# Kernel tuning notes

Measured on AMD Instinct MI355X. Metric: run time of the kernel, lower is better.

## Reference

```python
import jax, jax.numpy as jnp
import numpy as np

B, S = 2, 512
HID, FEAT = 768, 256
H, W = 512, 512
NUM_CLASSES = 9
BN_EPS = 1e-5


def setup_inputs() -> dict:
    key = jax.random.key(0)
    ks = jax.random.split(key, 20)
    hidden_states = jax.random.normal(ks[0], (B, S, HID), dtype=jnp.float32)
    # bbox in LayoutLM 0..1000 space, guaranteed x2>x1, y2>y1 for realistic coverage
    x1 = jax.random.randint(ks[1], (B, S), 0, 880)
    y1 = jax.random.randint(ks[2], (B, S), 0, 880)
    bw = jax.random.randint(ks[3], (B, S), 8, 120)
    bh = jax.random.randint(ks[4], (B, S), 8, 120)
    bbox = jnp.stack([x1, y1, jnp.minimum(x1 + bw, 1000), jnp.minimum(y1 + bh, 1000)], axis=-1).astype(jnp.int32)
    attention_mask = jnp.ones((B, S), dtype=jnp.int32)
    w_init = lambda k, shp: jax.random.normal(k, shp, dtype=jnp.float32) * 0.02
    return {
        "hidden_states": hidden_states,
        "bbox": bbox,
        "attention_mask": attention_mask,
        "proj_w": w_init(ks[5], (HID, FEAT)),
        "proj_b": jnp.zeros((FEAT,), jnp.float32),
        "conv1_w": w_init(ks[6], (128, FEAT, 3, 3)),
        "conv1_b": jnp.zeros((128,), jnp.float32),
        "bn1_g": jnp.ones((128,), jnp.float32),
        "bn1_b": jnp.zeros((128,), jnp.float32),
        "bn1_m": jnp.zeros((128,), jnp.float32),
        "bn1_v": jnp.ones((128,), jnp.float32),
        "conv2_w": w_init(ks[7], (64, 128, 3, 3)),
        "conv2_b": jnp.zeros((64,), jnp.float32),
        "bn2_g": jnp.ones((64,), jnp.float32),
        "bn2_b": jnp.zeros((64,), jnp.float32),
        "bn2_m": jnp.zeros((64,), jnp.float32),
        "bn2_v": jnp.ones((64,), jnp.float32),
        "conv3_w": w_init(ks[8], (NUM_CLASSES, 64, 1, 1)),
        "conv3_b": jnp.zeros((NUM_CLASSES,), jnp.float32),
    }


def _conv(x, w, b, pad):
    y = jax.lax.conv_general_dilated(x, w, (1, 1), [(pad, pad), (pad, pad)],
                                     dimension_numbers=("NCHW", "OIHW", "NCHW"))
    return y + b[None, :, None, None]


def _bn(x, g, b, m, v):
    scale = g / jnp.sqrt(v + BN_EPS)
    return (x - m[None, :, None, None]) * scale[None, :, None, None] + b[None, :, None, None]


def reference(hidden_states, bbox, attention_mask, proj_w, proj_b,
              conv1_w, conv1_b, bn1_g, bn1_b, bn1_m, bn1_v,
              conv2_w, conv2_b, bn2_g, bn2_b, bn2_m, bn2_v,
              conv3_w, conv3_b):
    features = hidden_states @ proj_w + proj_b  # [B,S,FEAT]

    # integer pixel coords, matching int(x * dim / 1000) truncation for x >= 0
    x1 = jnp.maximum((bbox[..., 0] * W) // 1000, 0)
    y1 = jnp.maximum((bbox[..., 1] * H) // 1000, 0)
    x2 = jnp.minimum((bbox[..., 2] * W) // 1000, W - 1)
    y2 = jnp.minimum((bbox[..., 3] * H) // 1000, H - 1)
    valid = (attention_mask == 1) & (jnp.arange(S) >= 1) & (x2 > x1) & (y2 > y1)  # [B,S]

    rows = jnp.arange(H)
    cols = jnp.arange(W)
    rows_in = (rows[None, None, :] >= y1[..., None]) & (rows[None, None, :] < y2[..., None])  # [B,S,H]
    cols_in = (cols[None, None, :] >= x1[..., None]) & (cols[None, None, :] < x2[..., None])  # [B,S,W]

    # sequential priority scatter: later tokens overwrite earlier ones
    def step(winner, xs):
        r, c, v, i = xs  # r:[B,H] c:[B,W] v:[B] i:scalar
        cov = v[:, None, None] & (r[:, :, None] & c[:, None, :])
        return jnp.where(cov, i, winner), None

    winner0 = jnp.zeros((B, H, W), jnp.int32)  # 0 == empty (token 0 is never valid)
    xs = (rows_in.transpose(1, 0, 2), cols_in.transpose(1, 0, 2),
          valid.T, jnp.arange(S, dtype=jnp.int32))
    winner, _ = jax.lax.scan(step, winner0, xs)  # [B,H,W]

    idx = winner.reshape(B, H * W)
    fm = jnp.take_along_axis(features, idx[:, :, None], axis=1)  # [B,HW,FEAT]
    fm = jnp.where((idx > 0)[:, :, None], fm, 0.0)
    feature_map = fm.reshape(B, H, W, FEAT).transpose(0, 3, 1, 2)  # [B,FEAT,H,W]

    x = jax.nn.relu(_bn(_conv(feature_map, conv1_w, conv1_b, 1), bn1_g, bn1_b, bn1_m, bn1_v))
    x = jax.nn.relu(_bn(_conv(x, conv2_w, conv2_b, 1), bn2_g, bn2_b, bn2_m, bn2_v))
    logits = _conv(x, conv3_w, conv3_b, 0)  # [B,NUM_CLASSES,H,W]
    return logits
```

## Files before the change

### kernel.cpp

```cpp
#include <hip/hip_runtime.h>
#include <hip/hip_bf16.h>

typedef __bf16 bf16x8 __attribute__((ext_vector_type(8)));
typedef float f32x4 __attribute__((ext_vector_type(4)));

#define HH 512
#define WW 512
#define NC 9
#define LDSB 25344
#define W3_OFF 62208
#define B3_OFF 64512

static __device__ __forceinline__ ushort f2bf(float x) {
  union { float f; unsigned u; } c; c.f = x;
  unsigned r = c.u + 0x7FFFu + ((c.u >> 16) & 1u);
  return (ushort)(r >> 16);
}

__global__ __launch_bounds__(256) void proj_gemm_kernel(
    const float* __restrict__ hs, const float* __restrict__ pw,
    const float* __restrict__ pb, float* __restrict__ feat) {
  __shared__ float As[16 * 132];
  __shared__ float4 Bs4[2048];
  int tid = threadIdx.x;
  int r0 = blockIdx.x * 16;
  int n0 = blockIdx.y * 64;
  int r = tid >> 4;
  int c4 = (tid & 15) << 2;
  float4 acc = *(const float4*)(pb + n0 + c4);
  for (int k0 = 0; k0 < 768; k0 += 128) {
    __syncthreads();
    #pragma unroll
    for (int i = 0; i < 8; ++i) {
      int idx = tid + i * 256;
      As[(idx >> 7) * 132 + (idx & 127)] =
          hs[(size_t)(r0 + (idx >> 7)) * 768 + k0 + (idx & 127)];
    }
    #pragma unroll
    for (int i = 0; i < 8; ++i) {
      int idx = tid + i * 256;
      Bs4[idx] = *(const float4*)(pw + (size_t)(k0 + (idx >> 4)) * 256 + n0 + ((idx & 15) << 2));
    }
    __syncthreads();
    const float* ar = As + r * 132;
    #pragma unroll 8
    for (int k = 0; k < 128; ++k) {
      float a = ar[k];
      float4 bv = Bs4[(k << 4) + (c4 >> 2)];
      acc.x = fmaf(a, bv.x, acc.x); acc.y = fmaf(a, bv.y, acc.y);
      acc.z = fmaf(a, bv.z, acc.z); acc.w = fmaf(a, bv.w, acc.w);
    }
  }
  *(float4*)(feat + (size_t)(r0 + r) * 256 + n0 + c4) = acc;
}

__global__ __launch_bounds__(64) void scatter_kernel(
    const int* __restrict__ bbox, const int* __restrict__ amask,
    int* __restrict__ winner) {
  int token = blockIdx.x;
  int b = token >> 9, s = token & 511;
  if (s == 0) return;
  const int* bb = bbox + (size_t)token * 4;
  int x1 = (bb[0] * 512) / 1000; if (x1 < 0) x1 = 0;
  int y1 = (bb[1] * 512) / 1000; if (y1 < 0) y1 = 0;
  int x2 = (bb[2] * 512) / 1000; if (x2 > 511) x2 = 511;
  int y2 = (bb[3] * 512) / 1000; if (y2 > 511) y2 = 511;
  if (amask[token] != 1 || x2 <= x1 || y2 <= y1) return;
  int lane = threadIdx.x;
  for (int yy = y1; yy < y2; ++yy) {
    int rowbase = (b << 18) + (yy << 9);
    for (int xx = x1 + lane; xx < x2; xx += 64)
      atomicMax(&winner[rowbase + xx], s);
  }
}

__global__ __launch_bounds__(256) void w1r_kernel(
    const float* __restrict__ w1, float* __restrict__ w1r) {
  int idx = blockIdx.x * 256 + threadIdx.x;
  int ic = idx / 1152, rem = idx - ic * 1152;
  int tap = rem >> 7, oc = rem & 127;
  w1r[idx] = w1[(size_t)oc * 2304 + ic * 9 + tap];
}

__global__ __launch_bounds__(256) void gtab_gemm_kernel(
    const float* __restrict__ feat, const float* __restrict__ w1r,
    float* __restrict__ G) {
  __shared__ float As[16 * 132];
  __shared__ float4 Bs4[2048];
  int tid = threadIdx.x;
  int r0 = blockIdx.x * 16;
  int n0 = blockIdx.y * 64;
  int r = tid >> 4;
  int c4 = (tid & 15) << 2;
  float4 acc = make_float4(0.f, 0.f, 0.f, 0.f);
  for (int k0 = 0; k0 < 256; k0 += 128) {
    __syncthreads();
    #pragma unroll
    for (int i = 0; i < 8; ++i) {
      int idx = tid + i * 256;
      As[(idx >> 7) * 132 + (idx & 127)] =
          feat[(size_t)(r0 + (idx >> 7)) * 256 + k0 + (idx & 127)];
    }
    #pragma unroll
    for (int i = 0; i < 8; ++i) {
      int idx = tid + i * 256;
      Bs4[idx] = *(const float4*)(w1r + (size_t)(k0 + (idx >> 4)) * 1152 + n0 + ((idx & 15) << 2));
    }
    __syncthreads();
    const float* ar = As + r * 132;
    #pragma unroll 8
    for (int k = 0; k < 128; ++k) {
      float a = ar[k];
      float4 bv = Bs4[(k << 4) + (c4 >> 2)];
      acc.x = fmaf(a, bv.x, acc.x); acc.y = fmaf(a, bv.y, acc.y);
      acc.z = fmaf(a, bv.z, acc.z); acc.w = fmaf(a, bv.w, acc.w);
    }
  }
  int row = r0 + r;
  if ((row & 511) == 0) acc = make_float4(0.f, 0.f, 0.f, 0.f);
  *(float4*)(G + (size_t)row * 1152 + n0 + c4) = acc;
}

__global__ __launch_bounds__(256) void gall_kernel(
    const float* __restrict__ G, float* __restrict__ Gall) {
  int idx = blockIdx.x * 256 + threadIdx.x;
  int row = idx >> 7, oc = idx & 127;
  const float* gr = G + (size_t)row * 1152 + oc;
  float s = 0.f;
  #pragma unroll
  for (int t = 0; t < 9; ++t) s += gr[t * 128];
  Gall[idx] = s;
}

__global__ __launch_bounds__(256) void w2t_kernel(
    const float* __restrict__ w2, ushort* __restrict__ w2t) {
  int oc = blockIdx.x;
  for (int k = threadIdx.x; k < 1152; k += 256) {
    int tap = k >> 7, ic = k & 127;
    w2t[(size_t)oc * 1152 + k] = f2bf(w2[(size_t)oc * 1152 + ic * 9 + tap]);
  }
}

__global__ __launch_bounds__(256) void conv1_gather_kernel(
    const int* __restrict__ winner,
    const float* __restrict__ G, const float* __restrict__ Gall,
    const float* __restrict__ cb, const float* __restrict__ g,
    const float* __restrict__ bt, const float* __restrict__ m,
    const float* __restrict__ v,
    ushort* __restrict__ buf1, size_t bstride, int b0, int hstart) {
  __shared__ float sscl[128], sshf[128];
  int tid = threadIdx.x;
  if (tid < 128) {
    float s = g[tid] * rsqrtf(v[tid] + 1e-5f);
    sscl[tid] = s;
    sshf[tid] = (cb[tid] - m[tid]) * s + bt[tid];
  }
  __syncthreads();
  int b = b0 + blockIdx.z;
  int px = blockIdx.x * 256 + tid;
  int r = px >> 9, w = px & 511;
  int h = hstart + r;
  ushort* dst = buf1 + (size_t)blockIdx.z * bstride + (size_t)px * 128;
  if (h < 0 || h >= HH) {
    uint4 z = make_uint4(0, 0, 0, 0);
    #pragma unroll
    for (int j = 0; j < 16; ++j) *(uint4*)(dst + j * 8) = z;
    return;
  }
  const int* wb = winner + (b << 18);
  int win[9];
  #pragma unroll
  for (int ky = 0; ky < 3; ++ky)
    #pragma unroll
    for (int kx = 0; kx < 3; ++kx) {
      int hp = h - 1 + ky, wp = w - 1 + kx;
      int s = 0;
      if (hp >= 0 && hp < HH && wp >= 0 && wp < WW) s = wb[(hp << 9) + wp];
      win[ky * 3 + kx] = s;
    }
  bool alleq = true;
  #pragma unroll
  for (int t = 1; t < 9; ++t) alleq = alleq && (win[t] == win[0]);

  if (alleq) {
    const float4* gp = (const float4*)(Gall + ((((size_t)b << 9) + win[0]) << 7));
    #pragma unroll
    for (int o8 = 0; o8 < 16; ++o8) {
      float4 a0 = gp[o8 * 2], a1 = gp[o8 * 2 + 1];
      const float* sc = &sscl[o8 * 8];
      const float* sh = &sshf[o8 * 8];
      union { ushort us[8]; uint4 v4; } pk;
      pk.us[0] = f2bf(fmaxf(fmaf(a0.x, sc[0], sh[0]), 0.f));
      pk.us[1] = f2bf(fmaxf(fmaf(a0.y, sc[1], sh[1]), 0.f));
      pk.us[2] = f2bf(fmaxf(fmaf(a0.z, sc[2], sh[2]), 0.f));
      pk.us[3] = f2bf(fmaxf(fmaf(a0.w, sc[3], sh[3]), 0.f));
      pk.us[4] = f2bf(fmaxf(fmaf(a1.x, sc[4], sh[4]), 0.f));
      pk.us[5] = f2bf(fmaxf(fmaf(a1.y, sc[5], sh[5]), 0.f));
      pk.us[6] = f2bf(fmaxf(fmaf(a1.z, sc[6], sh[6]), 0.f));
      pk.us[7] = f2bf(fmaxf(fmaf(a1.w, sc[7], sh[7]), 0.f));
      *(uint4*)(dst + o8 * 8) = pk.v4;
    }
  } else {
    size_t off[9];
    #pragma unroll
    for (int t = 0; t < 9; ++t)
      off[t] = ((size_t)((b << 9) + win[t])) * 1152 + t * 128;
    #pragma unroll
    for (int o8 = 0; o8 < 16; ++o8) {
      float4 a0 = make_float4(0, 0, 0, 0), a1 = a0;
      #pragma unroll
      for (int t = 0; t < 9; ++t) {
        const float4* gp = (const float4*)(G + off[t] + o8 * 8);
        float4 g0 = gp[0], g1 = gp[1];
        a0.x += g0.x; a0.y += g0.y; a0.z += g0.z; a0.w += g0.w;
        a1.x += g1.x; a1.y += g1.y; a1.z += g1.z; a1.w += g1.w;
      }
      const float* sc = &sscl[o8 * 8];
      const float* sh = &sshf[o8 * 8];
      union { ushort us[8]; uint4 v4; } pk;
      pk.us[0] = f2bf(fmaxf(fmaf(a0.x, sc[0], sh[0]), 0.f));
      pk.us[1] = f2bf(fmaxf(fmaf(a0.y, sc[1], sh[1]), 0.f));
      pk.us[2] = f2bf(fmaxf(fmaf(a0.z, sc[2], sh[2]), 0.f));
      pk.us[3] = f2bf(fmaxf(fmaf(a0.w, sc[3], sh[3]), 0.f));
      pk.us[4] = f2bf(fmaxf(fmaf(a1.x, sc[4], sh[4]), 0.f));
      pk.us[5] = f2bf(fmaxf(fmaf(a1.y, sc[5], sh[5]), 0.f));
      pk.us[6] = f2bf(fmaxf(fmaf(a1.z, sc[6], sh[6]), 0.f));
      pk.us[7] = f2bf(fmaxf(fmaf(a1.w, sc[7], sh[7]), 0.f));
      *(uint4*)(dst + o8 * 8) = pk.v4;
    }
  }
}

__global__ __launch_bounds__(256) void conv2_mfma_kernel(
    const ushort* __restrict__ buf1, const ushort* __restrict__ w2t,
    const float* __restrict__ cb, const float* __restrict__ g,
    const float* __restrict__ bt, const float* __restrict__ m_,
    const float* __restrict__ v_,
    const float* __restrict__ w3, const float* __restrict__ b3,
    float* __restrict__ out, size_t bstride, int b0, int hs0, int SR) {
  __shared__ uint4 lds4[4035];
  char* smem = (char*)lds4;
  int tid = threadIdx.x;
  int w0 = blockIdx.x * 64;
  int oh0 = blockIdx.y * 4;
  int b = b0 + blockIdx.z;
  const ushort* B1 = buf1 + (size_t)blockIdx.z * bstride;
  int wv = tid >> 6, lane = tid & 63;
  int l15 = lane & 15, l4 = lane >> 4;

  float scl[4], shf[4];
  #pragma unroll
  for (int nf = 0; nf < 4; ++nf) {
    int oc = nf * 16 + l15;
    float s = g[oc] * rsqrtf(v_[oc] + 1e-5f);
    scl[nf] = s;
    shf[nf] = (cb[oc] - m_[oc]) * s + bt[oc];
  }

  int aaddr[4][3];
  #pragma unroll
  for (int mf = 0; mf < 4; ++mf)
    #pragma unroll
    for (int kx = 0; kx < 3; ++kx) {
      int col = mf * 16 + l15 + kx;
      aaddr[mf][kx] = wv * 4224 + (col << 6) + ((l4 << 4) ^ (((col >> 1) & 3) << 4));
    }
  int baddr[4];
  #pragma unroll
  for (int nf = 0; nf < 4; ++nf) {
    int n = nf * 16 + l15;
    baddr[nf] = LDSB + (n << 6) + ((l4 << 4) ^ (((n >> 1) & 3) << 4));
  }

  f32x4 acc[4][4];
  #pragma unroll
  for (int mf = 0; mf < 4; ++mf)
    #pragma unroll
    for (int nf = 0; nf < 4; ++nf)
      acc[mf][nf] = (f32x4){0.f, 0.f, 0.f, 0.f};

  int bn = tid >> 2, bslot = tid & 3;
  int bd = LDSB + (bn << 6) + ((bslot << 4) ^ (((bn >> 1) & 3) << 4));

  for (int chunk = 0; chunk < 4; ++chunk) {
    int ic0 = chunk * 32;
    __syncthreads();
    uint4 av0, av1, av2, av3, av4, av5, av6;
    int ad0, ad1, ad2, ad3, ad4, ad5, ad6 = 0;
    av6 = make_uint4(0, 0, 0, 0);
#define ADEC(II, AV, AD) { \
      int i_ = (II); int slot = i_ & 3; int q = i_ >> 2; \
      int r_ = (q * 993) >> 16; int c_ = q - r_ * 66; \
      int wg = w0 - 1 + c_; \
      AD = ((r_ * 66 + c_) << 6) + ((slot << 4) ^ (((c_ >> 1) & 3) << 4)); \
      AV = make_uint4(0, 0, 0, 0); \
      if (wg >= 0 && wg < 512) \
        AV = *(const uint4*)(B1 + ((((size_t)(oh0 + r_)) << 9) + wg) * 128 + ic0 + slot * 8); \
    }
    ADEC(tid, av0, ad0);
    ADEC(tid + 256, av1, ad1);
    ADEC(tid + 512, av2, ad2);
    ADEC(tid + 768, av3, ad3);
    ADEC(tid + 1024, av4, ad4);
    ADEC(tid + 1280, av5, ad5);
    if (tid < 48) ADEC(tid + 1536, av6, ad6);
#undef ADEC
    uint4 bv[9];
    const ushort* wsrc = w2t + (size_t)bn * 1152 + ic0 + bslot * 8;
    #pragma unroll
    for (int j = 0; j < 9; ++j) bv[j] = *(const uint4*)(wsrc + j * 128);

    *(uint4*)(smem + ad0) = av0;
    *(uint4*)(smem + ad1) = av1;
    *(uint4*)(smem + ad2) = av2;
    *(uint4*)(smem + ad3) = av3;
    *(uint4*)(smem + ad4) = av4;
    *(uint4*)(smem + ad5) = av5;
    if (tid < 48) *(uint4*)(smem + ad6) = av6;
    #pragma unroll
    for (int j = 0; j < 9; ++j) *(uint4*)(smem + bd + j * 4096) = bv[j];
    __syncthreads();

    #pragma unroll
    for (int ky = 0; ky < 3; ++ky) {
      #pragma unroll
      for (int kx = 0; kx < 3; ++kx) {
        const int tap = ky * 3 + kx;
        bf16x8 bf0 = *(const bf16x8*)(smem + baddr[0] + tap * 4096);
        bf16x8 bf1 = *(const bf16x8*)(smem + baddr[1] + tap * 4096);
        bf16x8 bf2 = *(const bf16x8*)(smem + baddr[2] + tap * 4096);
        bf16x8 bf3 = *(const bf16x8*)(smem + baddr[3] + tap * 4096);
        #pragma unroll
        for (int mf = 0; mf < 4; ++mf) {
          bf16x8 af = *(const bf16x8*)(smem + aaddr[mf][kx] + ky * 4224);
          acc[mf][0] = __builtin_amdgcn_mfma_f32_16x16x32_bf16(af, bf0, acc[mf][0], 0, 0, 0);
          acc[mf][1] = __builtin_amdgcn_mfma_f32_16x16x32_bf16(af, bf1, acc[mf][1], 0, 0, 0);
          acc[mf][2] = __builtin_amdgcn_mfma_f32_16x16x32_bf16(af, bf2, acc[mf][2], 0, 0, 0);
          acc[mf][3] = __builtin_amdgcn_mfma_f32_16x16x32_bf16(af, bf3, acc[mf][3], 0, 0, 0);
        }
      }
    }
  }

  __syncthreads();
  #pragma unroll
  for (int half = 0; half < 2; ++half) {
    if (half) __syncthreads();
    if ((wv >> 1) == half) {
      #pragma unroll
      for (int mf = 0; mf < 4; ++mf)
        #pragma unroll
        for (int nf = 0; nf < 4; ++nf)
          #pragma unroll
          for (int rr = 0; rr < 4; ++rr) {
            int px = (wv & 1) * 64 + mf * 16 + l4 * 4 + rr;
            int oc = nf * 16 + l15;
            float val = fmaxf(fmaf(acc[mf][nf][rr], scl[nf], shf[nf]), 0.f);
            *(float*)(smem + (px * 66 + oc) * 4) = val;
          }
    }
    if (half == 0 && tid >= 128) {
      int idx = tid - 128;
      #pragma unroll
      for (int j = 0; j < 2; ++j) {
        int ii = idx + j * 128;
        if (ii < 144) *(uint4*)(smem + W3_OFF + ii * 16) = *(const uint4*)(w3 + ii * 4);
      }
      if (idx < NC) *(float*)(smem + B3_OFF + idx * 4) = b3[idx];
    }
    __syncthreads();
    if (tid < 128) {
      const float* w3f = (const float*)(smem + W3_OFF);
      const float* b3f = (const float*)(smem + B3_OFF);
      float a9[NC];
      #pragma unroll
      for (int c = 0; c < NC; ++c) a9[c] = b3f[c];
      #pragma unroll 8
      for (int j = 0; j < 32; ++j) {
        float2 xv = *(const float2*)(smem + (tid * 66 + 2 * j) * 4);
        #pragma unroll
        for (int c = 0; c < NC; ++c)
          a9[c] = fmaf(xv.x, w3f[c * 64 + 2 * j], fmaf(xv.y, w3f[c * 64 + 2 * j + 1], a9[c]));
      }
      int h = hs0 + oh0 + half * 2 + (tid >> 6);
      int w = w0 + (tid & 63);
      size_t base = ((size_t)b * NC) * 262144 + (size_t)h * 512 + w;
      #pragma unroll
      for (int c = 0; c < NC; ++c) out[base + (size_t)c * 262144] = a9[c];
    }
  }
}

extern "C" void kernel_launch(void* const* d_in, const int* in_sizes, int n_in,
                              void* d_out, int out_size, void* d_ws, size_t ws_size,
                              hipStream_t stream) {
  const float* hs  = (const float*)d_in[0];
  const int* bbox  = (const int*)d_in[1];
  const int* amask = (const int*)d_in[2];
  const float* pw  = (const float*)d_in[3];
  const float* pb  = (const float*)d_in[4];
  const float* w1  = (const float*)d_in[5];
  const float* c1b = (const float*)d_in[6];
  const float* g1  = (const float*)d_in[7];
  const float* b1  = (const float*)d_in[8];
  const float* m1  = (const float*)d_in[9];
  const float* v1  = (const float*)d_in[10];
  const float* w2  = (const float*)d_in[11];
  const float* c2b = (const float*)d_in[12];
  const float* g2  = (const float*)d_in[13];
  const float* b2  = (const float*)d_in[14];
  const float* m2  = (const float*)d_in[15];
  const float* v2  = (const float*)d_in[16];
  const float* w3  = (const float*)d_in[17];
  const float* b3  = (const float*)d_in[18];
  float* out = (float*)d_out;

  char* wsb = (char*)d_ws;
  float*  feat   = (float*)(wsb + 0);
  int*    winner = (int*)(wsb + 1048576);
  float*  G      = (float*)(wsb + 3145728);
  float*  Gall   = (float*)(wsb + 7864320);
  float*  w1r    = (float*)(wsb + 8388608);
  ushort* w2t    = (ushort*)(wsb + 10485760);
  ushort* buf1   = (ushort*)(wsb + 10747904);

  int SR = 512;
  while (SR > 32) {
    if (10747904 + (size_t)(SR + 2) * 131072 <= ws_size) break;
    SR >>= 1;
  }
  size_t b1s = (size_t)(SR + 2) * 65536;
  int NB = (SR == 512 && ws_size >= 10747904 + 4 * b1s) ? 2 : 1;

  hipMemsetAsync(winner, 0, 2097152, stream);
  proj_gemm_kernel<<<dim3(64, 4), 256, 0, stream>>>(hs, pw, pb, feat);
  scatter_kernel<<<1024, 64, 0, stream>>>(bbox, amask, winner);
  w1r_kernel<<<1152, 256, 0, stream>>>(w1, w1r);
  gtab_gemm_kernel<<<dim3(64, 18), 256, 0, stream>>>(feat, w1r, G);
  gall_kernel<<<512, 256, 0, stream>>>(G, Gall);
  w2t_kernel<<<64, 256, 0, stream>>>(w2, w2t);

  if (NB == 2) {
    conv1_gather_kernel<<<dim3((SR + 2) * 512 / 256, 1, 2), 256, 0, stream>>>(
        winner, G, Gall, c1b, g1, b1, m1, v1, buf1, b1s, 0, -1);
    conv2_mfma_kernel<<<dim3(8, SR / 4, 2), 256, 0, stream>>>(
        buf1, w2t, c2b, g2, b2, m2, v2, w3, b3, out, b1s, 0, 0, SR);
  } else {
    int nstripes = 512 / SR;
    for (int b = 0; b < 2; ++b) {
      for (int s = 0; s < nstripes; ++s) {
        int hs0 = s * SR;
        conv1_gather_kernel<<<dim3((SR + 2) * 512 / 256, 1, 1), 256, 0, stream>>>(
            winner, G, Gall, c1b, g1, b1, m1, v1, buf1, (size_t)0, b, hs0 - 1);
        conv2_mfma_kernel<<<dim3(8, SR / 4, 1), 256, 0, stream>>>(
            buf1, w2t, c2b, g2, b2, m2, v2, w3, b3, out, (size_t)0, b, hs0, SR);
      }
    }
  }
}
```

Baseline: 266.0 us.

## Prefetch next conv2 input chunk into registers during MFMA compute

Restructures the conv2 channel-chunk loop so global loads for the next 32-channel chunk are issued right after the current chunk is written to LDS. Those loads then overlap the MFMA work instead of sitting exposed at the top of each iteration. Address and bounds computations are hoisted out of the loop. __syncthreads is replaced with a custom barrier that waits only on lgkmcnt, so outstanding global loads are not forced to complete at the barrier. This raises register pressure (16 uint4 held live alongside the accumulators), which may hurt occupancy.

```diff
diff --git a/kernel.cpp b/kernel.cpp
--- a/kernel.cpp
+++ b/kernel.cpp
@@ -10,6 +10,8 @@
 #define LDSB 25344
 #define W3_OFF 62208
 #define B3_OFF 64512
+
+#define BARRIER() asm volatile("s_waitcnt lgkmcnt(0)\n\ts_barrier" ::: "memory")
 
 static __device__ __forceinline__ ushort f2bf(float x) {
   union { float f; unsigned u; } c; c.f = x;
@@ -279,47 +281,46 @@
     for (int nf = 0; nf < 4; ++nf)
       acc[mf][nf] = (f32x4){0.f, 0.f, 0.f, 0.f};
 
+  const ushort* asrc[7]; int aad[7]; bool ainr[7];
+  #pragma unroll
+  for (int i = 0; i < 7; ++i) {
+    int i_ = tid + i * 256;
+    bool act = (i < 6) || (tid < 48);
+    int slot = i_ & 3, q = i_ >> 2;
+    int r_ = (q * 993) >> 16, c_ = q - r_ * 66;
+    int wg = w0 - 1 + c_;
+    aad[i] = ((r_ * 66 + c_) << 6) + ((slot << 4) ^ (((c_ >> 1) & 3) << 4));
+    ainr[i] = act && (wg >= 0) && (wg < 512);
+    asrc[i] = B1 + ((((size_t)(oh0 + r_)) << 9) + (size_t)(wg < 0 ? 0 : wg)) * 128 + slot * 8;
+  }
   int bn = tid >> 2, bslot = tid & 3;
   int bd = LDSB + (bn << 6) + ((bslot << 4) ^ (((bn >> 1) & 3) << 4));
-
-  for (int chunk = 0; chunk < 4; ++chunk) {
-    int ic0 = chunk * 32;
-    __syncthreads();
-    uint4 av0, av1, av2, av3, av4, av5, av6;
-    int ad0, ad1, ad2, ad3, ad4, ad5, ad6 = 0;
-    av6 = make_uint4(0, 0, 0, 0);
-#define ADEC(II, AV, AD) { \
-      int i_ = (II); int slot = i_ & 3; int q = i_ >> 2; \
-      int r_ = (q * 993) >> 16; int c_ = q - r_ * 66; \
-      int wg = w0 - 1 + c_; \
-      AD = ((r_ * 66 + c_) << 6) + ((slot << 4) ^ (((c_ >> 1) & 3) << 4)); \
-      AV = make_uint4(0, 0, 0, 0); \
-      if (wg >= 0 && wg < 512) \
-        AV = *(const uint4*)(B1 + ((((size_t)(oh0 + r_)) << 9) + wg) * 128 + ic0 + slot * 8); \
-    }
-    ADEC(tid, av0, ad0);
-    ADEC(tid + 256, av1, ad1);
-    ADEC(tid + 512, av2, ad2);
-    ADEC(tid + 768, av3, ad3);
-    ADEC(tid + 1024, av4, ad4);
-    ADEC(tid + 1280, av5, ad5);
-    if (tid < 48) ADEC(tid + 1536, av6, ad6);
-#undef ADEC
-    uint4 bv[9];
-    const ushort* wsrc = w2t + (size_t)bn * 1152 + ic0 + bslot * 8;
-    #pragma unroll
-    for (int j = 0; j < 9; ++j) bv[j] = *(const uint4*)(wsrc + j * 128);
-
-    *(uint4*)(smem + ad0) = av0;
-    *(uint4*)(smem + ad1) = av1;
-    *(uint4*)(smem + ad2) = av2;
-    *(uint4*)(smem + ad3) = av3;
-    *(uint4*)(smem + ad4) = av4;
-    *(uint4*)(smem + ad5) = av5;
-    if (tid < 48) *(uint4*)(smem + ad6) = av6;
+  const ushort* wsrc = w2t + (size_t)bn * 1152 + bslot * 8;
+
+  uint4 av[7]; uint4 bv[9];
+  #pragma unroll
+  for (int i = 0; i < 7; ++i)
+    av[i] = ainr[i] ? *(const uint4*)(asrc[i]) : make_uint4(0, 0, 0, 0);
+  #pragma unroll
+  for (int j = 0; j < 9; ++j) bv[j] = *(const uint4*)(wsrc + j * 128);
+
+  #pragma unroll
+  for (int c = 0; c < 4; ++c) {
+    BARRIER();
+    #pragma unroll
+    for (int i = 0; i < 6; ++i) *(uint4*)(smem + aad[i]) = av[i];
+    if (tid < 48) *(uint4*)(smem + aad[6]) = av[6];
     #pragma unroll
     for (int j = 0; j < 9; ++j) *(uint4*)(smem + bd + j * 4096) = bv[j];
-    __syncthreads();
+    if (c < 3) {
+      const int icn = (c + 1) * 32;
+      #pragma unroll
+      for (int i = 0; i < 7; ++i)
+        av[i] = ainr[i] ? *(const uint4*)(asrc[i] + icn) : make_uint4(0, 0, 0, 0);
+      #pragma unroll
+      for (int j = 0; j < 9; ++j) bv[j] = *(const uint4*)(wsrc + icn + j * 128);
+    }
+    BARRIER();
 
     #pragma unroll
     for (int ky = 0; ky < 3; ++ky) {
```

Result: slower. 314.3 us (+18.2%).
